# Kernel optimization log

Hardware: AMD Instinct MI355X
Metric: run time of the kernel (lower is better)

## Reference

```python
import jax, jax.numpy as jnp
import numpy as np

EPS = 1e-08
N_CODECS = 1024

def setup_inputs() -> dict:
    key = jax.random.key(0)
    indices = jax.random.randint(key, (16, 1048576), 0, N_CODECS, dtype=jnp.int64 if jax.config.jax_enable_x64 else jnp.int32)
    return {"indices": indices}

def reference(indices) -> jnp.ndarray:
    # Faithful to: encodings = eq(arange[:,None], flat[None,:]); probs = mean(encodings, dim=1)
    # mean of one-hot over N == count/N, so use a histogram (bincount) instead of the
    # O(n_codecs x N) boolean matrix.
    flat = indices.reshape(-1)
    counts = jnp.bincount(flat, length=N_CODECS)  # [n_codecs]
    probs = counts.astype(jnp.float32) / flat.shape[0]
    perplexity = jnp.exp(-jnp.sum(probs * jnp.log(probs + EPS)))
    return perplexity
```

## Files before the change

### kernel.cpp

```cpp
#include <hip/hip_runtime.h>
#include <hip/hip_bf16.h>

#define N_CODECS 1024
#define EPS 1e-8f
#define HIST_BLOCKS 1024
#define CHUNKS 16

__global__ void __launch_bounds__(256) hist_partial_kernel(
        const int* __restrict__ idx,
        unsigned int* __restrict__ gpart,
        int n4) {
    __shared__ unsigned int lcounts[N_CODECS];
    for (int i = threadIdx.x; i < N_CODECS; i += 256) lcounts[i] = 0u;
    __syncthreads();

    const int4* __restrict__ idx4 = (const int4*)idx;
    int stride = gridDim.x * 256;
    for (int i = blockIdx.x * 256 + threadIdx.x; i < n4; i += stride) {
        int4 v = idx4[i];
        atomicAdd(&lcounts[v.x], 1u);
        atomicAdd(&lcounts[v.y], 1u);
        atomicAdd(&lcounts[v.z], 1u);
        atomicAdd(&lcounts[v.w], 1u);
    }
    __syncthreads();

    unsigned int* __restrict__ mypart = gpart + (size_t)blockIdx.x * N_CODECS;
    #pragma unroll
    for (int i = 0; i < N_CODECS / 256; ++i) {
        int b = i * 256 + threadIdx.x;
        mypart[b] = lcounts[b];
    }
}

__global__ void __launch_bounds__(256) reduce_kernel(
        const unsigned int* __restrict__ gpart,
        unsigned int* __restrict__ p2) {
    int c = blockIdx.x >> 2;
    int q = blockIdx.x & 3;
    int bin = q * 256 + threadIdx.x;

    const unsigned int* __restrict__ base = gpart + (size_t)(c * 64) * N_CODECS + bin;
    unsigned int s0 = 0, s1 = 0, s2 = 0, s3 = 0;
    #pragma unroll 4
    for (int k = 0; k < 64; k += 4) {
        s0 += base[(size_t)(k + 0) * N_CODECS];
        s1 += base[(size_t)(k + 1) * N_CODECS];
        s2 += base[(size_t)(k + 2) * N_CODECS];
        s3 += base[(size_t)(k + 3) * N_CODECS];
    }
    p2[c * N_CODECS + bin] = s0 + s1 + s2 + s3;
}

__global__ void __launch_bounds__(1024) finalize_kernel(
        const unsigned int* __restrict__ p2,
        float* __restrict__ out,
        float invN) {
    int t = threadIdx.x;
    unsigned int cnt = 0;
    #pragma unroll
    for (int c = 0; c < CHUNKS; ++c) cnt += p2[c * N_CODECS + t];

    float p = (float)cnt * invN;
    float term = p * logf(p + EPS);

    #pragma unroll
    for (int off = 32; off > 0; off >>= 1) term += __shfl_down(term, off, 64);

    __shared__ float wsum[16];
    int wave = t >> 6;
    int lane = t & 63;
    if (lane == 0) wsum[wave] = term;
    __syncthreads();

    if (wave == 0) {
        float s = (lane < 16) ? wsum[lane] : 0.0f;
        #pragma unroll
        for (int off = 8; off > 0; off >>= 1) s += __shfl_down(s, off, 64);
        if (lane == 0) out[0] = expf(-s);
    }
}

extern "C" void kernel_launch(void* const* d_in, const int* in_sizes, int n_in,
                              void* d_out, int out_size, void* d_ws, size_t ws_size,
                              hipStream_t stream) {
    const int* indices = (const int*)d_in[0];
    int n = in_sizes[0];
    float* out = (float*)d_out;

    unsigned int* gpart = (unsigned int*)d_ws;
    unsigned int* p2    = gpart + (size_t)HIST_BLOCKS * N_CODECS;

    int n4 = n >> 2;

    hist_partial_kernel<<<HIST_BLOCKS, 256, 0, stream>>>(indices, gpart, n4);
    reduce_kernel<<<CHUNKS * 4, 256, 0, stream>>>(gpart, p2);
    finalize_kernel<<<1, 1024, 0, stream>>>(p2, out, 1.0f / (float)n);
}
```

Baseline: 94.06 us.

## Pack partial histograms to 16-bit and fuse reduce with finalize via last-block

Each histogram block now packs two 16-bit bin counts into one 32-bit word, halving the partial-histogram writes and the reads in the reduction. The reduce and finalize kernels are merged into one kernel: the last block to finish, found through an atomic counter, computes the entropy and perplexity, which removes one kernel launch. The reduce grid drops from 64 to 16 blocks, each doing more work, and fast __logf/__expf intrinsics replace the precise calls. Risks are 16-bit overflow if a block's count for a bin exceeds 65535, and lower parallelism in the reduction.

```diff
diff --git a/kernel.cpp b/kernel.cpp
--- a/kernel.cpp
+++ b/kernel.cpp
@@ -6,12 +6,16 @@
 #define HIST_BLOCKS 1024
 #define CHUNKS 16
 
+
 __global__ void __launch_bounds__(256) hist_partial_kernel(
         const int* __restrict__ idx,
-        unsigned int* __restrict__ gpart,
+        unsigned int* __restrict__ gpart_u32,
+        unsigned int* __restrict__ done,
         int n4) {
     __shared__ unsigned int lcounts[N_CODECS];
+    #pragma unroll
     for (int i = threadIdx.x; i < N_CODECS; i += 256) lcounts[i] = 0u;
+    if (blockIdx.x == 0 && threadIdx.x == 0) *done = 0u;
     __syncthreads();
 
     const int4* __restrict__ idx4 = (const int4*)idx;
@@ -25,60 +29,69 @@
     }
     __syncthreads();
 
-    unsigned int* __restrict__ mypart = gpart + (size_t)blockIdx.x * N_CODECS;
+    unsigned int* __restrict__ mypart = gpart_u32 + (size_t)blockIdx.x * (N_CODECS / 2);
     #pragma unroll
-    for (int i = 0; i < N_CODECS / 256; ++i) {
-        int b = i * 256 + threadIdx.x;
-        mypart[b] = lcounts[b];
+    for (int i = 0; i < 2; ++i) {
+        int c = i * 256 + threadIdx.x;
+        mypart[c] = lcounts[2 * c] | (lcounts[2 * c + 1] << 16);
     }
 }
 
-__global__ void __launch_bounds__(256) reduce_kernel(
-        const unsigned int* __restrict__ gpart,
-        unsigned int* __restrict__ p2) {
-    int c = blockIdx.x >> 2;
-    int q = blockIdx.x & 3;
-    int bin = q * 256 + threadIdx.x;
-
-    const unsigned int* __restrict__ base = gpart + (size_t)(c * 64) * N_CODECS + bin;
-    unsigned int s0 = 0, s1 = 0, s2 = 0, s3 = 0;
-    #pragma unroll 4
-    for (int k = 0; k < 64; k += 4) {
-        s0 += base[(size_t)(k + 0) * N_CODECS];
-        s1 += base[(size_t)(k + 1) * N_CODECS];
-        s2 += base[(size_t)(k + 2) * N_CODECS];
-        s3 += base[(size_t)(k + 3) * N_CODECS];
-    }
-    p2[c * N_CODECS + bin] = s0 + s1 + s2 + s3;
-}
-
-__global__ void __launch_bounds__(1024) finalize_kernel(
-        const unsigned int* __restrict__ p2,
+__global__ void __launch_bounds__(256) reduce_finalize_kernel(
+        const unsigned int* __restrict__ gpart_u32,
+        unsigned int* __restrict__ p2,
+        unsigned int* __restrict__ done,
         float* __restrict__ out,
         float invN) {
-    int t = threadIdx.x;
-    unsigned int cnt = 0;
+    const int c = blockIdx.x;
+    const int t = threadIdx.x;
+    const unsigned int* __restrict__ base = gpart_u32 + (size_t)(c * 64) * 512;
+
+    unsigned int s0lo = 0, s0hi = 0, s1lo = 0, s1hi = 0;
+    #pragma unroll 4
+    for (int k = 0; k < 64; ++k) {
+        unsigned int v0 = base[(size_t)k * 512 + t];
+        unsigned int v1 = base[(size_t)k * 512 + 256 + t];
+        s0lo += v0 & 0xFFFFu;  s0hi += v0 >> 16;
+        s1lo += v1 & 0xFFFFu;  s1hi += v1 >> 16;
+    }
+    p2[c * N_CODECS + 2 * t]           = s0lo;
+    p2[c * N_CODECS + 2 * t + 1]       = s0hi;
+    p2[c * N_CODECS + 512 + 2 * t]     = s1lo;
+    p2[c * N_CODECS + 512 + 2 * t + 1] = s1hi;
+
+    __threadfence();
+    __syncthreads();
+
+    __shared__ bool amLast;
+    if (t == 0) {
+        unsigned int prev = atomicAdd(done, 1u);
+        amLast = (prev == (unsigned int)(gridDim.x - 1));
+    }
+    __syncthreads();
+    if (!amLast) return;
+
+    __threadfence();
+
+    float local = 0.0f;
     #pragma unroll
-    for (int c = 0; c < CHUNKS; ++c) cnt += p2[c * N_CODECS + t];
-
-    float p = (float)cnt * invN;
-    float term = p * logf(p + EPS);
+    for (int i = 0; i < N_CODECS / 256; ++i) {
+        int b = i * 256 + t;
+        unsigned int cnt = 0;
+        #pragma unroll
+        for (int ch = 0; ch < CHUNKS; ++ch) cnt += p2[ch * N_CODECS + b];
+        float p = (float)cnt * invN;
+        local += p * __logf(p + EPS);
+    }
 
     #pragma unroll
-    for (int off = 32; off > 0; off >>= 1) term += __shfl_down(term, off, 64);
+    for (int off = 32; off > 0; off >>= 1) local += __shfl_down(local, off, 64);
 
-    __shared__ float wsum[16];
-    int wave = t >> 6;
-    int lane = t & 63;
-    if (lane == 0) wsum[wave] = term;
+    __shared__ float wsum[4];
+    int wave = t >> 6, lane = t & 63;
+    if (lane == 0) wsum[wave] = local;
     __syncthreads();
-
-    if (wave == 0) {
-        float s = (lane < 16) ? wsum[lane] : 0.0f;
-        #pragma unroll
-        for (int off = 8; off > 0; off >>= 1) s += __shfl_down(s, off, 64);
-        if (lane == 0) out[0] = expf(-s);
-    }
+    if (t == 0) out[0] = __expf(-(wsum[0] + wsum[1] + wsum[2] + wsum[3]));
 }
 
 extern "C" void kernel_launch(void* const* d_in, const int* in_sizes, int n_in,
@@ -89,11 +102,12 @@
     float* out = (float*)d_out;
 
     unsigned int* gpart = (unsigned int*)d_ws;
-    unsigned int* p2    = gpart + (size_t)HIST_BLOCKS * N_CODECS;
+    unsigned int* p2    = gpart + (size_t)HIST_BLOCKS * (N_CODECS / 2);
+    unsigned int* done  = p2 + (size_t)CHUNKS * N_CODECS;
 
     int n4 = n >> 2;
 
-    hist_partial_kernel<<<HIST_BLOCKS, 256, 0, stream>>>(indices, gpart, n4);
-    reduce_kernel<<<CHUNKS * 4, 256, 0, stream>>>(gpart, p2);
-    finalize_kernel<<<1, 1024, 0, stream>>>(p2, out, 1.0f / (float)n);
+    hist_partial_kernel<<<HIST_BLOCKS, 256, 0, stream>>>(indices, gpart, done, n4);
+    reduce_finalize_kernel<<<CHUNKS, 256, 0, stream>>>(gpart, p2, done, out,
+                                                       1.0f / (float)n);
 }
```

After: 97.56 us. +3.7%, slower.
